# Kernel optimization log

Measured on AMD Instinct MI355X. Metric: run time of the kernel, lower is better.

The kernel has to match this reference:

```python
import jax, jax.numpy as jnp
import numpy as np
import math

# Static config derived from init_kwargs
B, L, D, H, NL = 256, 256, 128, 2, 2
E = D // H                       # 64
F = L // 2 + 1                   # 129 rfft bins
SR = 0.6                         # sample_ratio (> 1/n_layers)
STEP = (F * (1.0 - SR)) // (NL - 1)          # 51.0, python float floor-div as in torch code
LEFTS = [int(F * (1.0 - SR) - k * STEP) for k in range(NL)]   # [51, 0]
RIGHTS = [int(F - k * STEP) for k in range(NL)]               # [129, 78]
TOPK = max(int(1 * math.log(L)), 1)          # factor=1 -> 5
NUM_TOTAL = 100000                           # user_num + item_num
SPATIAL_RATIO = 0.1
INV_SQRT_E = 1.0 / math.sqrt(E)
INV_SQRT_2 = 1.0 / math.sqrt(2.0)


def setup_inputs() -> dict:
    key = jax.random.key(0)
    ks = jax.random.split(key, 12)
    s = 0.05
    return {
        "paths": jax.random.randint(ks[0], (B, L), 0, NUM_TOTAL),
        "lengths": jax.random.randint(ks[1], (B,), 1, L + 1),
        "degrees": jax.random.randint(ks[2], (B,), 0, 64),
        "training": 1,
        "ego_emb": jax.random.normal(ks[3], (NUM_TOTAL + 1, D), jnp.float32) * s,
        "pos_emb": jax.random.normal(ks[4], (L, D), jnp.float32) * s,
        "Wq": jax.random.normal(ks[5], (NL, D, D), jnp.float32) * s,
        "Wk": jax.random.normal(ks[6], (NL, D, D), jnp.float32) * s,
        "Wv": jax.random.normal(ks[7], (NL, D, D), jnp.float32) * s,
        "Wp": jax.random.normal(ks[8], (NL, D, D), jnp.float32) * s,
        "F1": jax.random.normal(ks[9], (NL, D, 2 * D), jnp.float32) * s,
        "F2": jax.random.normal(ks[10], (NL, 2 * D, D), jnp.float32) * s,
    }


def _hybrid_attention(k, x, mask, Wq, Wk, Wv, Wp):
    # project and split heads: [B,H,E,L]
    def proj(W):
        return (x @ W).reshape(B, L, H, E).transpose(0, 2, 3, 1)
    q, kk, v = proj(Wq), proj(Wk), proj(Wv)
    qf = jnp.fft.rfft(q, axis=-1)   # [B,H,E,F] complex
    kf = jnp.fft.rfft(kk, axis=-1)
    vf = jnp.fft.rfft(v, axis=-1)
    l, r = LEFTS[k], RIGHTS[k]
    # frequency-band attention: band-limited cross-correlation (scatter back == zero-pad)
    res = qf[..., l:r] * jnp.conj(kf[..., l:r])
    box = jnp.zeros(qf.shape, dtype=res.dtype).at[..., l:r].set(res)
    corr = jnp.fft.irfft(box, n=L, axis=-1)          # [B,H,E,L]
    mean_value = jnp.mean(corr, axis=(1, 2))         # [B,L]
    # training branch: global topk delays (shared across batch), roll-based aggregation
    _, delays = jax.lax.top_k(jnp.mean(mean_value, axis=0), TOPK)   # [TOPK]
    weights = mean_value[:, delays]                  # [B,TOPK]
    tmp_corr = jax.nn.softmax(weights, axis=-1)      # [B,TOPK]
    # roll(v, -d) along time == gather at (t + d) % L
    idx = (jnp.arange(L)[None, :] + delays[:, None]) % L            # [TOPK,L]
    gathered = v[:, :, :, idx]                       # [B,H,E,TOPK,L]
    freq = jnp.einsum('bhetl,bt->bhel', gathered, tmp_corr)
    freq = freq.transpose(0, 3, 1, 2).reshape(B, L, D)
    # dual-domain: time attention on band-limited signals (std=True -> same band)
    def band_ifft(f):
        padded = jnp.zeros(f.shape, dtype=f.dtype).at[..., l:r].set(f[..., l:r])
        return jnp.fft.irfft(padded, n=L, axis=-1).transpose(0, 1, 3, 2)   # [B,H,L,E]
    qt, kt, vt = band_ifft(qf), band_ifft(kf), band_ifft(vf)
    scores = jnp.einsum('bhqe,bhke->bhqk', qt, kt) * INV_SQRT_E + mask
    att = jax.nn.softmax(scores, axis=-1)
    spatial = jnp.einsum('bhqk,bhke->bhqe', att, vt).transpose(0, 2, 1, 3).reshape(B, L, D)
    out = (1.0 - SPATIAL_RATIO) * freq + SPATIAL_RATIO * spatial
    return out @ Wp + x


def reference(paths, lengths, degrees, training, ego_emb, pos_emb, Wq, Wk, Wv, Wp, F1, F2):
    del degrees, training  # degrees unused; training branch baked in (training=True)
    x = ego_emb[paths] + pos_emb[None, :, :]         # [B,L,D]
    m = (paths < NUM_TOTAL).astype(jnp.float32)
    mask = ((1.0 - m) * -10000.0)[:, None, None, :]  # [B,1,1,L]
    for k in range(NL):
        a = _hybrid_attention(k, x, mask, Wq[k], Wk[k], Wv[k], Wp[k])
        h = a @ F1[k]
        h = h * 0.5 * (1.0 + jax.lax.erf(h * INV_SQRT_2))   # exact GELU
        x = h @ F2[k]
    # gather last valid position per sequence
    return x[jnp.arange(B), lengths - 1]             # [B,D]
```

## Files before the change

kernel.cpp:

```cpp
#include <hip/hip_runtime.h>
#include <math.h>

#define Bn 256
#define Ln 256
#define Dn 128
#define Hn 2
#define En 64
#define NLn 2
#define TOPKn 5
#define NUM_TOTALn 100000
#define BLD (Bn*Ln*Dn)
#define WT_LAYER 147456

using frag_ab = __attribute__((ext_vector_type(8))) short;
using frag_cd = __attribute__((ext_vector_type(4))) float;

__device__ inline short f2bf(float f) {
    union { float f; unsigned u; } c; c.f = f;
    unsigned r = (c.u + 0x7FFFu + ((c.u >> 16) & 1u)) >> 16;
    return (short)r;
}
__device__ inline float bf2f(short s) {
    union { unsigned u; float f; } c; c.u = ((unsigned)(unsigned short)s) << 16;
    return c.f;
}

__global__ void beacon_kernel(float* out, float v) { out[0] = v; }

__global__ __launch_bounds__(256) void build_G_kernel(short* __restrict__ G) {
    int k = blockIdx.x, t = blockIdx.y, s = threadIdx.x;
    int d = (t - s) & 255;
    int f1 = (k == 0) ? 51 : 1;
    int f2 = (k == 0) ? 127 : 77;
    float acc;
    if (d == 0) {
        acc = 2.0f * (float)(f2 - f1 + 1);
    } else {
        const float c = 3.14159265358979323846f / 256.0f;
        int ahi = (d * (2 * f2 + 1)) & 511;
        int alo = (d * (2 * f1 - 1)) & 511;
        acc = (sinf(c * (float)ahi) - sinf(c * (float)alo)) / sinf(c * (float)d);
    }
    acc += (k == 0) ? ((d & 1) ? -1.0f : 1.0f)
                    : 1.0f;
    G[((size_t)k * 256 + t) * 256 + s] = f2bf(acc * (1.0f / 256.0f));
}

__global__ __launch_bounds__(256) void build_x_kernel(const int* __restrict__ paths,
                                                      const float* __restrict__ ego,
                                                      const float* __restrict__ pos,
                                                      short* __restrict__ x) {
    int base = (blockIdx.x * 256 + threadIdx.x) * 4;
    int d = base & 127;
    int bl = base >> 7;
    int t = bl & 255;
    float4 e = *(const float4*)(ego + (size_t)paths[bl] * Dn + d);
    float4 p = *(const float4*)(pos + t * Dn + d);
    short4 s;
    s.x = f2bf(e.x + p.x); s.y = f2bf(e.y + p.y);
    s.z = f2bf(e.z + p.z); s.w = f2bf(e.w + p.w);
    *(short4*)&x[base] = s;
}

__global__ __launch_bounds__(256) void wtrans_all_kernel(
        const float* __restrict__ Wq, const float* __restrict__ Wk,
        const float* __restrict__ Wv, const float* __restrict__ Wp,
        const float* __restrict__ F1, const float* __restrict__ F2,
        short* __restrict__ Wt) {
    int z = blockIdx.y;
    int idx = blockIdx.x * 256 + threadIdx.x;
    short* WtL = Wt + (size_t)z * WT_LAYER;
    if (idx < 65536) {
        int which = idx >> 14, local = idx & 16383;
        const float* src = (which == 0) ? Wq : (which == 1) ? Wk
                         : (which == 2) ? Wv : Wp;
        float scale = (which == 3) ? 0.1f : 1.0f;
        int n = local & 127, k = local >> 7;
        WtL[(which << 14) + n * 128 + k] = f2bf(scale * src[(size_t)z * 16384 + local]);
    } else if (idx < 98304) {
        int local = idx - 65536;
        int n = local & 255, k = local >> 8;
        WtL[65536 + n * 128 + k] = f2bf(F1[(size_t)z * 32768 + local]);
    } else {
        int local = idx - 98304;
        int n = local & 127, k = local >> 7;
        WtL[98304 + n * 256 + k] = f2bf(F2[(size_t)z * 32768 + local]);
    }
}

template<bool BT_FAST, bool GELU_EPI>
__global__ __launch_bounds__(256)
void mfma_gemm_kernel(const short* A, const short* Bp, short* C, const short* R,
                      int K, int lda, int ldb, int ldc, int ldr,
                      long long sA, long long sB, long long sC, long long sR,
                      long long sCsplit, float alpha, float beta) {
    int bz = blockIdx.z;
    A += (size_t)bz * sA; C += (size_t)bz * sC;
    if (R) R += (size_t)bz * sR;
    const short* Bt = Bp + (size_t)bz * sB;
    const int m0 = blockIdx.x * 128, n0 = blockIdx.y * 128;
    int n0c = n0;
    if (sCsplit) { C += (size_t)blockIdx.y * sCsplit; n0c = 0; }
    __shared__ short As[128 * 40];
    __shared__ short Bs[128 * 40];
    int tid = threadIdx.x;
    int lane = tid & 63, wave = tid >> 6;
    int wr = (wave >> 1) * 64, wc = (wave & 1) * 64;
    int l15 = lane & 15, qd = lane >> 4;

    frag_cd zero4 = {0.f, 0.f, 0.f, 0.f};
    frag_cd acc[4][4];
    #pragma unroll
    for (int i = 0; i < 4; i++)
        #pragma unroll
        for (int j = 0; j < 4; j++) acc[i][j] = zero4;

    int arow = tid >> 1, acg = (tid & 1) * 16;
    int bnrow = tid >> 1, bcg = (tid & 1) * 16;
    int bkk = tid & 31, bnb = (tid >> 5) * 16;

    int4 pa0, pa1, pb0, pb1;
    {
        const short* ap = A + (size_t)(m0 + arow) * lda + acg;
        pa0 = *(const int4*)ap; pa1 = *(const int4*)(ap + 8);
        if (BT_FAST) {
            const short* bp = Bt + (size_t)(n0 + bnrow) * ldb + bcg;
            pb0 = *(const int4*)bp; pb1 = *(const int4*)(bp + 8);
        } else {
            const short* bp = Bt + (size_t)bkk * ldb + n0 + bnb;
            pb0 = *(const int4*)bp; pb1 = *(const int4*)(bp + 8);
        }
    }

    for (int k0 = 0; k0 < K; k0 += 32) {
        __syncthreads();
        *(int4*)&As[arow * 40 + acg] = pa0;
        *(int4*)&As[arow * 40 + acg + 8] = pa1;
        if (BT_FAST) {
            *(int4*)&Bs[bnrow * 40 + bcg] = pb0;
            *(int4*)&Bs[bnrow * 40 + bcg + 8] = pb1;
        } else {
            short tmp[16];
            *(int4*)&tmp[0] = pb0; *(int4*)&tmp[8] = pb1;
            #pragma unroll
            for (int i = 0; i < 16; i++) Bs[(bnb + i) * 40 + bkk] = tmp[i];
        }
        __syncthreads();
        if (k0 + 32 < K) {
            const short* ap = A + (size_t)(m0 + arow) * lda + k0 + 32 + acg;
            pa0 = *(const int4*)ap; pa1 = *(const int4*)(ap + 8);
            if (BT_FAST) {
                const short* bp = Bt + (size_t)(n0 + bnrow) * ldb + k0 + 32 + bcg;
                pb0 = *(const int4*)bp; pb1 = *(const int4*)(bp + 8);
            } else {
                const short* bp = Bt + (size_t)(k0 + 32 + bkk) * ldb + n0 + bnb;
                pb0 = *(const int4*)bp; pb1 = *(const int4*)(bp + 8);
            }
        }
        frag_ab af[4], bf[4];
        #pragma unroll
        for (int ms = 0; ms < 4; ms++)
            af[ms] = *(frag_ab*)&As[(wr + ms * 16 + l15) * 40 + qd * 8];
        #pragma unroll
        for (int ns = 0; ns < 4; ns++)
            bf[ns] = *(frag_ab*)&Bs[(wc + ns * 16 + l15) * 40 + qd * 8];
        #pragma unroll
        for (int ms = 0; ms < 4; ms++)
            #pragma unroll
            for (int ns = 0; ns < 4; ns++)
                acc[ms][ns] = __builtin_amdgcn_mfma_f32_16x16x32_bf16(
                    bf[ns], af[ms], acc[ms][ns], 0, 0, 0);
    }
    #pragma unroll
    for (int ms = 0; ms < 4; ms++) {
        int m = m0 + wr + ms * 16 + l15;
        #pragma unroll
        for (int ns = 0; ns < 4; ns++) {
            int nb = wc + ns * 16 + qd * 4;
            float v[4];
            #pragma unroll
            for (int r = 0; r < 4; r++) v[r] = alpha * acc[ms][ns][r];
            if (R) {
                short4 r4 = *(const short4*)&R[(size_t)m * ldr + n0 + nb];
                v[0] += beta * bf2f(r4.x); v[1] += beta * bf2f(r4.y);
                v[2] += beta * bf2f(r4.z); v[3] += beta * bf2f(r4.w);
            }
            if (GELU_EPI) {
                #pragma unroll
                for (int r = 0; r < 4; r++)
                    v[r] = v[r] * 0.5f * (1.0f + erff(v[r] * 0.70710678118654752f));
            }
            short4 o;
            o.x = f2bf(v[0]); o.y = f2bf(v[1]); o.z = f2bf(v[2]); o.w = f2bf(v[3]);
            *(short4*)&C[(size_t)m * ldc + n0c + nb] = o;
        }
    }
}

static inline void mgemm(hipStream_t s, const short* A, const short* B, short* C,
                         const short* R, int M, int N, int K,
                         int lda, int ldb, int ldc, int ldr,
                         long long sA, long long sB, long long sC, long long sR,
                         int batch, float alpha, float beta, bool btFast, bool gelu,
                         long long sCsplit = 0) {
    dim3 grid(M / 128, N / 128, batch), block(256);
    if (btFast) {
        if (gelu) mfma_gemm_kernel<true, true ><<<grid, block, 0, s>>>(A, B, C, R, K, lda, ldb, ldc, ldr, sA, sB, sC, sR, sCsplit, alpha, beta);
        else      mfma_gemm_kernel<true, false><<<grid, block, 0, s>>>(A, B, C, R, K, lda, ldb, ldc, ldr, sA, sB, sC, sR, sCsplit, alpha, beta);
    } else {
        if (gelu) mfma_gemm_kernel<false, true ><<<grid, block, 0, s>>>(A, B, C, R, K, lda, ldb, ldc, ldr, sA, sB, sC, sR, sCsplit, alpha, beta);
        else      mfma_gemm_kernel<false, false><<<grid, block, 0, s>>>(A, B, C, R, K, lda, ldb, ldc, ldr, sA, sB, sC, sR, sCsplit, alpha, beta);
    }
}

__global__ __launch_bounds__(512)
void filtproj_kernel(const short* __restrict__ G, const short* __restrict__ x,
                     const short* __restrict__ W, short* __restrict__ q) {
    int b = blockIdx.x;
    __shared__ short As[256 * 40];
    __shared__ short Bs[128 * 40];
    __shared__ short xf[256 * 136];
    int tid = threadIdx.x;
    int lane = tid & 63, wave = tid >> 6;
    int wr = (wave & 3) * 64, wc = (wave >> 2) * 64;
    int l15 = lane & 15, qd = lane >> 4;
    const short* xb = x + ((size_t)b << 15);

    frag_cd zero4 = {0.f, 0.f, 0.f, 0.f};
    frag_cd acc[4][4];
    #pragma unroll
    for (int i = 0; i < 4; i++)
        #pragma unroll
        for (int j = 0; j < 4; j++) acc[i][j] = zero4;

    int arow = tid >> 1, acg = (tid & 1) * 16;
    int bkk = tid & 31, bnb = (tid >> 5) * 16;

    int4 pa0, pa1, pb0, pb1;
    {
        const short* ap = G + (size_t)arow * 256 + acg;
        pa0 = *(const int4*)ap; pa1 = *(const int4*)(ap + 8);
        if (tid < 256) {
            const short* bp = xb + (size_t)bkk * 128 + bnb;
            pb0 = *(const int4*)bp; pb1 = *(const int4*)(bp + 8);
        }
    }
    for (int k0 = 0; k0 < 256; k0 += 32) {
        __syncthreads();
        *(int4*)&As[arow * 40 + acg] = pa0;
        *(int4*)&As[arow * 40 + acg + 8] = pa1;
        if (tid < 256) {
            short tmp[16];
            *(int4*)&tmp[0] = pb0; *(int4*)&tmp[8] = pb1;
            #pragma unroll
            for (int i = 0; i < 16; i++) Bs[(bnb + i) * 40 + bkk] = tmp[i];
        }
        __syncthreads();
        if (k0 + 32 < 256) {
            const short* ap = G + (size_t)arow * 256 + k0 + 32 + acg;
            pa0 = *(const int4*)ap; pa1 = *(const int4*)(ap + 8);
            if (tid < 256) {
                const short* bp = xb + (size_t)(k0 + 32 + bkk) * 128 + bnb;
                pb0 = *(const int4*)bp; pb1 = *(const int4*)(bp + 8);
            }
        }
        frag_ab af[4], bf[4];
        #pragma unroll
        for (int ms = 0; ms < 4; ms++)
            af[ms] = *(frag_ab*)&As[(wr + ms * 16 + l15) * 40 + qd * 8];
        #pragma unroll
        for (int ns = 0; ns < 4; ns++)
            bf[ns] = *(frag_ab*)&Bs[(wc + ns * 16 + l15) * 40 + qd * 8];
        #pragma unroll
        for (int ms = 0; ms < 4; ms++)
            #pragma unroll
            for (int ns = 0; ns < 4; ns++)
                acc[ms][ns] = __builtin_amdgcn_mfma_f32_16x16x32_bf16(
                    bf[ns], af[ms], acc[ms][ns], 0, 0, 0);
    }
    #pragma unroll
    for (int ms = 0; ms < 4; ms++) {
        int m = wr + ms * 16 + l15;
        #pragma unroll
        for (int ns = 0; ns < 4; ns++) {
            int nb = wc + ns * 16 + qd * 4;
            short4 o;
            o.x = f2bf(acc[ms][ns][0]); o.y = f2bf(acc[ms][ns][1]);
            o.z = f2bf(acc[ms][ns][2]); o.w = f2bf(acc[ms][ns][3]);
            *(short4*)&xf[m * 136 + nb] = o;
        }
    }

    int brow = tid >> 2, bcg = (tid & 3) * 8;
    #pragma unroll 1
    for (int y = 0; y < 3; y++) {
        const short* Bt = W + y * 16384;
        #pragma unroll
        for (int i = 0; i < 4; i++)
            #pragma unroll
            for (int j = 0; j < 4; j++) acc[i][j] = zero4;
        int4 pb = *(const int4*)(Bt + (size_t)brow * 128 + bcg);
        for (int k0 = 0; k0 < 128; k0 += 32) {
            __syncthreads();
            *(int4*)&Bs[brow * 40 + bcg] = pb;
            __syncthreads();
            if (k0 + 32 < 128)
                pb = *(const int4*)(Bt + (size_t)brow * 128 + k0 + 32 + bcg);
            frag_ab af[4], bf[4];
            #pragma unroll
            for (int ms = 0; ms < 4; ms++)
                af[ms] = *(frag_ab*)&xf[(wr + ms * 16 + l15) * 136 + k0 + qd * 8];
            #pragma unroll
            for (int ns = 0; ns < 4; ns++)
                bf[ns] = *(frag_ab*)&Bs[(wc + ns * 16 + l15) * 40 + qd * 8];
            #pragma unroll
            for (int ms = 0; ms < 4; ms++)
                #pragma unroll
                for (int ns = 0; ns < 4; ns++)
                    acc[ms][ns] = __builtin_amdgcn_mfma_f32_16x16x32_bf16(
                        bf[ns], af[ms], acc[ms][ns], 0, 0, 0);
        }
        short* Cy = q + (size_t)y * BLD + ((size_t)b << 15);
        #pragma unroll
        for (int ms = 0; ms < 4; ms++) {
            int m = wr + ms * 16 + l15;
            #pragma unroll
            for (int ns = 0; ns < 4; ns++) {
                int nb = wc + ns * 16 + qd * 4;
                short4 o;
                o.x = f2bf(acc[ms][ns][0]); o.y = f2bf(acc[ms][ns][1]);
                o.z = f2bf(acc[ms][ns][2]); o.w = f2bf(acc[ms][ns][3]);
                *(short4*)&Cy[(size_t)m * 128 + nb] = o;
            }
        }
    }
}

__global__ __launch_bounds__(512)
void amix_ffn_kernel(const short* __restrict__ x, const short* __restrict__ q,
                     const short* __restrict__ W,
                     const float* __restrict__ tc, const int* __restrict__ delays,
                     short* __restrict__ xout) {
    int b = blockIdx.x;
    __shared__ short aL[256 * 132];
    __shared__ short hA[256 * 132];
    __shared__ short Bs[128 * 40];
    short* As = hA;
    int tid = threadIdx.x;
    int lane = tid & 63, wave = tid >> 6;
    int wr = (wave & 3) * 64, wc = (wave >> 2) * 64;
    int l15 = lane & 15, qd = lane >> 4;
    const short* xb = x + ((size_t)b << 15);

    float wj[TOPKn]; int dj[TOPKn];
    #pragma unroll
    for (int j = 0; j < TOPKn; j++) {
        wj[j] = tc[b * TOPKn + j];
        dj[j] = delays[j];
    }

    frag_cd zero4 = {0.f, 0.f, 0.f, 0.f};
    frag_cd acc[4][4];
    #pragma unroll
    for (int i = 0; i < 4; i++)
        #pragma unroll
        for (int j = 0; j < 4; j++) acc[i][j] = zero4;

    int arow = tid >> 1, acg = (tid & 1) * 16;
    int brow = tid >> 2, bcg = (tid & 3) * 8;

    {
        const short* Bt = W + 131072;
        int4 pb0 = *(const int4*)(Bt + (size_t)brow * 128 + bcg);
        for (int k0 = 0; k0 < 128; k0 += 32) {
            __syncthreads();
            #pragma unroll
            for (int c = 0; c < 2; c++) {
                int col = k0 + acg + c * 8;
                float m8[8] = {0.f, 0.f, 0.f, 0.f, 0.f, 0.f, 0.f, 0.f};
                #pragma unroll
                for (int j = 0; j < TOPKn; j++) {
                    frag_ab v = *(const frag_ab*)(xb + (((arow + dj[j]) & 255) << 7) + col);
                    #pragma unroll
                    for (int i = 0; i < 8; i++) m8[i] += wj[j] * bf2f(v[i]);
                }
                frag_ab o;
                #pragma unroll
                for (int i = 0; i < 8; i++) o[i] = f2bf(m8[i]);
                *(frag_ab*)&As[arow * 40 + acg + c * 8] = o;
            }
            *(int4*)&Bs[brow * 40 + bcg] = pb0;
            __syncthreads();
            if (k0 + 32 < 128)
                pb0 = *(const int4*)(Bt + (size_t)brow * 128 + k0 + 32 + bcg);
            frag_ab af[4], bf[4];
            #pragma unroll
            for (int ms = 0; ms < 4; ms++)
                af[ms] = *(frag_ab*)&As[(wr + ms * 16 + l15) * 40 + qd * 8];
            #pragma unroll
            for (int ns = 0; ns < 4; ns++)
                bf[ns] = *(frag_ab*)&Bs[(wc + ns * 16 + l15) * 40 + qd * 8];
            #pragma unroll
            for (int ms = 0; ms < 4; ms++)
                #pragma unroll
                for (int ns = 0; ns < 4; ns++)
                    acc[ms][ns] = __builtin_amdgcn_mfma_f32_16x16x32_bf16(
                        bf[ns], af[ms], acc[ms][ns], 0, 0, 0);
        }
    }
    {
        const short* A2 = q + ((size_t)b << 15);
        const short* Bt = W + 49152;
        int4 pa0, pa1, pb0;
        {
            const short* ap = A2 + (size_t)arow * 128 + acg;
            pa0 = *(const int4*)ap; pa1 = *(const int4*)(ap + 8);
            pb0 = *(const int4*)(Bt + (size_t)brow * 128 + bcg);
        }
        for (int k0 = 0; k0 < 128; k0 += 32) {
            __syncthreads();
            *(int4*)&As[arow * 40 + acg] = pa0;
            *(int4*)&As[arow * 40 + acg + 8] = pa1;
            *(int4*)&Bs[brow * 40 + bcg] = pb0;
            __syncthreads();
            if (k0 + 32 < 128) {
                const short* ap = A2 + (size_t)arow * 128 + k0 + 32 + acg;
                pa0 = *(const int4*)ap; pa1 = *(const int4*)(ap + 8);
                pb0 = *(const int4*)(Bt + (size_t)brow * 128 + k0 + 32 + bcg);
            }
            frag_ab af[4], bf[4];
            #pragma unroll
            for (int ms = 0; ms < 4; ms++)
                af[ms] = *(frag_ab*)&As[(wr + ms * 16 + l15) * 40 + qd * 8];
            #pragma unroll
            for (int ns = 0; ns < 4; ns++)
                bf[ns] = *(frag_ab*)&Bs[(wc + ns * 16 + l15) * 40 + qd * 8];
            #pragma unroll
            for (int ms = 0; ms < 4; ms++)
                #pragma unroll
                for (int ns = 0; ns < 4; ns++)
                    acc[ms][ns] = __builtin_amdgcn_mfma_f32_16x16x32_bf16(
                        bf[ns], af[ms], acc[ms][ns], 0, 0, 0);
        }
    }
    __syncthreads();
    #pragma unroll
    for (int ms = 0; ms < 4; ms++) {
        int m = wr + ms * 16 + l15;
        #pragma unroll
        for (int ns = 0; ns < 4; ns++) {
            int nb = wc + ns * 16 + qd * 4;
            short4 r4 = *(const short4*)&xb[(size_t)m * 128 + nb];
            float v[4];
            v[0] = acc[ms][ns][0] + bf2f(r4.x);
            v[1] = acc[ms][ns][1] + bf2f(r4.y);
            v[2] = acc[ms][ns][2] + bf2f(r4.z);
            v[3] = acc[ms][ns][3] + bf2f(r4.w);
            short4 o;
            o.x = f2bf(v[0]); o.y = f2bf(v[1]); o.z = f2bf(v[2]); o.w = f2bf(v[3]);
            *(short4*)&aL[m * 132 + nb] = o;
        }
    }
    __syncthreads();

    const short* F1T = W + 65536;
    const short* F2T = W + 98304;
    frag_cd xacc[4][4];
    #pragma unroll
    for (int i = 0; i < 4; i++)
        #pragma unroll
        for (int j = 0; j < 4; j++) xacc[i][j] = zero4;

    #pragma unroll 1
    for (int half = 0; half < 2; half++) {
        const short* B1 = F1T + (size_t)(half * 128) * 128;
        frag_cd hacc[4][4];
        #pragma unroll
        for (int i = 0; i < 4; i++)
            #pragma unroll
            for (int j = 0; j < 4; j++) hacc[i][j] = zero4;
        int4 pb = *(const int4*)(B1 + (size_t)brow * 128 + bcg);
        for (int k0 = 0; k0 < 128; k0 += 32) {
            __syncthreads();
            *(int4*)&Bs[brow * 40 + bcg] = pb;
            __syncthreads();
            if (k0 + 32 < 128)
                pb = *(const int4*)(B1 + (size_t)brow * 128 + k0 + 32 + bcg);
            frag_ab af[4], bf[4];
            #pragma unroll
            for (int ms = 0; ms < 4; ms++)
                af[ms] = *(frag_ab*)&aL[(wr + ms * 16 + l15) * 132 + k0 + qd * 8];
            #pragma unroll
            for (int ns = 0; ns < 4; ns++)
                bf[ns] = *(frag_ab*)&Bs[(wc + ns * 16 + l15) * 40 + qd * 8];
            #pragma unroll
            for (int ms = 0; ms < 4; ms++)
                #pragma unroll
                for (int ns = 0; ns < 4; ns++)
                    hacc[ms][ns] = __builtin_amdgcn_mfma_f32_16x16x32_bf16(
                        bf[ns], af[ms], hacc[ms][ns], 0, 0, 0);
        }
        __syncthreads();
        #pragma unroll
        for (int ms = 0; ms < 4; ms++) {
            int m = wr + ms * 16 + l15;
            #pragma unroll
            for (int ns = 0; ns < 4; ns++) {
                int nb = wc + ns * 16 + qd * 4;
                float v[4];
                #pragma unroll
                for (int r = 0; r < 4; r++) {
                    float t = hacc[ms][ns][r];
                    v[r] = t * 0.5f * (1.0f + erff(t * 0.70710678118654752f));
                }
                short4 o;
                o.x = f2bf(v[0]); o.y = f2bf(v[1]);
                o.z = f2bf(v[2]); o.w = f2bf(v[3]);
                *(short4*)&hA[m * 132 + nb] = o;
            }
        }
        __syncthreads();

        int4 pb2 = *(const int4*)(F2T + (size_t)brow * 256 + half * 128 + bcg);
        for (int k0 = 0; k0 < 128; k0 += 32) {
            __syncthreads();
            *(int4*)&Bs[brow * 40 + bcg] = pb2;
            __syncthreads();
            if (k0 + 32 < 128)
                pb2 = *(const int4*)(F2T + (size_t)brow * 256 + half * 128 + k0 + 32 + bcg);
            frag_ab af[4], bf[4];
            #pragma unroll
            for (int ms = 0; ms < 4; ms++)
                af[ms] = *(frag_ab*)&hA[(wr + ms * 16 + l15) * 132 + k0 + qd * 8];
            #pragma unroll
            for (int ns = 0; ns < 4; ns++)
                bf[ns] = *(frag_ab*)&Bs[(wc + ns * 16 + l15) * 40 + qd * 8];
            #pragma unroll
            for (int ms = 0; ms < 4; ms++)
                #pragma unroll
                for (int ns = 0; ns < 4; ns++)
                    xacc[ms][ns] = __builtin_amdgcn_mfma_f32_16x16x32_bf16(
                        bf[ns], af[ms], xacc[ms][ns], 0, 0, 0);
        }
    }
    short* xo = xout + ((size_t)b << 15);
    #pragma unroll
    for (int ms = 0; ms < 4; ms++) {
        int m = wr + ms * 16 + l15;
        #pragma unroll
        for (int ns = 0; ns < 4; ns++) {
            int nb = wc + ns * 16 + qd * 4;
            short4 o;
            o.x = f2bf(xacc[ms][ns][0]); o.y = f2bf(xacc[ms][ns][1]);
            o.z = f2bf(xacc[ms][ns][2]); o.w = f2bf(xacc[ms][ns][3]);
            *(short4*)&xo[(size_t)m * 128 + nb] = o;
        }
    }
}

__global__ __launch_bounds__(512, 4) void attn_kernel(short* q,
        const short* __restrict__ kb, const short* __restrict__ vf,
        const int* __restrict__ paths, float* __restrict__ mv2) {
    int h = blockIdx.x, b = blockIdx.y;
    __shared__ short SB[256 * 72];
    __shared__ short ks[64 * 72];
    __shared__ short vT[80 * 72];
    __shared__ float masks[256];
    __shared__ float mvpart[512];
    int tid = threadIdx.x;
    int lane = tid & 63, wave = tid >> 6;
    int l15 = lane & 15, qd = lane >> 4;
    if (tid < 256) masks[tid] = (paths[b * 256 + tid] < NUM_TOTALn) ? 0.0f : -10000.0f;
    {
        int e0 = tid * 2;
        #pragma unroll
        for (int i = 0; i < 2; i++) {
            int e = e0 + i;
            int row = 64 + (e >> 6), col = e & 63;
            vT[row * 72 + col] = (row == 64) ? (short)0x3F80 : (short)0;
        }
    }
    short* qg = q + ((size_t)b << 15) + (size_t)h * 64;
    const short* kg = kb + ((size_t)b << 15) + (size_t)h * 64;
    const short* vg = vf + ((size_t)b << 15) + (size_t)h * 64;

    #pragma unroll
    for (int p = 0; p < 4; p++) {
        int chunk = p * 512 + tid;
        int r = chunk >> 3, cb = (chunk & 7) * 8;
        *(frag_ab*)&SB[r * 72 + cb] = *(const frag_ab*)(qg + (size_t)r * 128 + cb);
    }
    __syncthreads();
    int myrow = wave * 32;
    frag_ab aq[2][2];
    #pragma unroll
    for (int mt = 0; mt < 2; mt++)
        #pragma unroll
        for (int hf = 0; hf < 2; hf++)
            aq[mt][hf] = *(frag_ab*)&SB[(myrow + mt * 16 + l15) * 72 + hf * 32 + qd * 8];

    frag_cd zero4 = {0.f, 0.f, 0.f, 0.f};
    frag_cd oacc[2][5];
    #pragma unroll
    for (int mt = 0; mt < 2; mt++)
        #pragma unroll
        for (int et = 0; et < 5; et++) oacc[mt][et] = zero4;
    float macc = 0.0f;
    int tau = tid & 255, half = tid >> 8;

    for (int jt = 0; jt < 4; jt++) {
        __syncthreads();
        {
            int r = tid >> 3, cb = (tid & 7) * 8;
            *(frag_ab*)&ks[r * 72 + cb] =
                *(const frag_ab*)(kg + (size_t)(jt * 64 + r) * 128 + cb);
            frag_ab v8 = *(const frag_ab*)(vg + (size_t)(jt * 64 + r) * 128 + cb);
            int swz = (((r >> 3) ^ (cb >> 3)) << 3) + (r & 7);
            #pragma unroll
            for (int i = 0; i < 8; i++) vT[(cb + i) * 72 + swz] = v8[i];
        }
        __syncthreads();
        #pragma unroll
        for (int mt = 0; mt < 2; mt++) {
            #pragma unroll
            for (int nt = 0; nt < 4; nt++) {
                frag_ab b0 = *(frag_ab*)&ks[(nt * 16 + l15) * 72 + qd * 8];
                frag_ab b1 = *(frag_ab*)&ks[(nt * 16 + l15) * 72 + 32 + qd * 8];
                frag_cd c = zero4;
                c = __builtin_amdgcn_mfma_f32_16x16x32_bf16(aq[mt][0], b0, c, 0, 0, 0);
                c = __builtin_amdgcn_mfma_f32_16x16x32_bf16(aq[mt][1], b1, c, 0, 0, 0);
                int keyLocal = nt * 16 + l15;
                #pragma unroll
                for (int r = 0; r < 4; r++) {
                    int row = myrow + mt * 16 + qd * 4 + r;
                    int tt = (row - jt * 64 - keyLocal) & 255;
                    SB[tt * 66 + keyLocal] = f2bf(c[r] * 0.125f);
                }
            }
        }
        __syncthreads();
        {
            const int* SD32 = (const int*)&SB[tau * 66 + half * 32];
            #pragma unroll
            for (int i = 0; i < 16; i++) {
                int pk = SD32[i];
                macc += bf2f((short)(pk & 0xFFFF)) + bf2f((short)(pk >> 16));
            }
        }
        #pragma unroll
        for (int mt = 0; mt < 2; mt++) {
            int row = myrow + mt * 16 + l15;
            #pragma unroll
            for (int hf = 0; hf < 2; hf++) {
                int kl0 = hf * 32 + qd * 8;
                frag_ab pfrag;
                #pragma unroll
                for (int j = 0; j < 8; j++) {
                    int kl = kl0 + j;
                    int tt = (row - jt * 64 - kl) & 255;
                    float s = bf2f(SB[tt * 66 + kl]);
                    pfrag[j] = f2bf(__expf(s + masks[jt * 64 + kl]));
                }
                #pragma unroll
                for (int et = 0; et < 5; et++) {
                    int e = et * 16 + l15;
                    int blk = (hf * 4 + qd) ^ ((e >> 3) & 7);
                    frag_ab bv = *(frag_ab*)&vT[e * 72 + (blk << 3)];
                    oacc[mt][et] = __builtin_amdgcn_mfma_f32_16x16x32_bf16(pfrag, bv, oacc[mt][et], 0, 0, 0);
                }
            }
        }
    }
    __syncthreads();
    mvpart[tid] = macc;
    __syncthreads();
    if (tid < 256)
        mv2[(size_t)h * 65536 + b * 256 + tid] =
            (mvpart[tid] + mvpart[tid + 256]) * 0.0625f;
    #pragma unroll
    for (int mt = 0; mt < 2; mt++) {
        #pragma unroll
        for (int r = 0; r < 4; r++) {
            float l = oacc[mt][4][r];
            l = __shfl(l, (lane & 48));
            float inv = 1.0f / l;
            int row = myrow + mt * 16 + qd * 4 + r;
            #pragma unroll
            for (int et = 0; et < 4; et++)
                qg[(size_t)row * 128 + et * 16 + l15] = f2bf(oacc[mt][et][r] * inv);
        }
    }
}

__global__ __launch_bounds__(256) void gm_reduce_kernel(const float* __restrict__ mv2,
                                                        float* __restrict__ gm) {
    int tau = blockIdx.x;
    int b = threadIdx.x;
    __shared__ float red[256];
    red[b] = mv2[b * 256 + tau] + mv2[65536 + b * 256 + tau];
    __syncthreads();
    for (int s = 128; s > 0; s >>= 1) { if (b < s) red[b] += red[b + s]; __syncthreads(); }
    if (b == 0) gm[tau] = red[0] * (1.0f / 256.0f);
}

__global__ __launch_bounds__(256) void topk_softmax_kernel(const float* __restrict__ gm,
                                                           const float* __restrict__ mv2,
                                                           int* __restrict__ delays,
                                                           float* __restrict__ tc) {
    __shared__ float vsh[4];
    __shared__ int ish[4];
    __shared__ int dsh[TOPKn];
    int tid = threadIdx.x;
    int lane = tid & 63, wave = tid >> 6;
    float v = gm[tid];
    for (int t = 0; t < TOPKn; t++) {
        float mv_ = v; int mi = tid;
        #pragma unroll
        for (int s = 32; s > 0; s >>= 1) {
            float v2 = __shfl_xor(mv_, s); int i2 = __shfl_xor(mi, s);
            if (v2 > mv_ || (v2 == mv_ && i2 < mi)) { mv_ = v2; mi = i2; }
        }
        if (lane == 0) { vsh[wave] = mv_; ish[wave] = mi; }
        __syncthreads();
        if (tid == 0) {
            float bv = vsh[0]; int bi = ish[0];
            #pragma unroll
            for (int w = 1; w < 4; w++)
                if (vsh[w] > bv || (vsh[w] == bv && ish[w] < bi)) { bv = vsh[w]; bi = ish[w]; }
            dsh[t] = bi; delays[t] = bi;
        }
        __syncthreads();
        if (tid == dsh[t]) v = -1e30f;
    }
    __syncthreads();
    int b = tid;
    float w[TOPKn];
    float m = -1e30f;
    #pragma unroll
    for (int j = 0; j < TOPKn; j++) {
        w[j] = mv2[b * 256 + dsh[j]] + mv2[65536 + b * 256 + dsh[j]];
        m = fmaxf(m, w[j]);
    }
    float ssum = 0.0f;
    #pragma unroll
    for (int j = 0; j < TOPKn; j++) { w[j] = expf(w[j] - m); ssum += w[j]; }
    #pragma unroll
    for (int j = 0; j < TOPKn; j++) tc[b * TOPKn + j] = w[j] / ssum;
}

__global__ __launch_bounds__(256) void gather_out_kernel(const short* __restrict__ x,
                                                         const int* __restrict__ lengths,
                                                         float* __restrict__ out) {
    int idx = blockIdx.x * 256 + threadIdx.x;
    int d = idx & 127;
    int b = idx >> 7;
    out[idx] = bf2f(x[((size_t)b << 15) + (size_t)(lengths[b] - 1) * Dn + d]);
}

extern "C" void kernel_launch(void* const* d_in, const int* in_sizes, int n_in,
                              void* d_out, int out_size, void* d_ws, size_t ws_size,
                              hipStream_t stream) {
    const int* paths    = (const int*)d_in[0];
    const int* lengths  = (const int*)d_in[1];
    const float* ego    = (const float*)d_in[4];
    const float* pos    = (const float*)d_in[5];
    const float* Wq     = (const float*)d_in[6];
    const float* Wk     = (const float*)d_in[7];
    const float* Wv     = (const float*)d_in[8];
    const float* Wp     = (const float*)d_in[9];
    const float* F1     = (const float*)d_in[10];
    const float* F2     = (const float*)d_in[11];
    float* out = (float*)d_out;

    const size_t need = (size_t)5 * BLD * 2 + 131072 * 2 + 131072 * 4
                        + 256 * 4 + 1280 * 4 + 16 * 4 + (size_t)NLn * WT_LAYER * 2;
    if (ws_size < need) {
        beacon_kernel<<<dim3(1), dim3(1), 0, stream>>>(out, (float)(ws_size >> 20));
        return;
    }

    short* x    = (short*)d_ws;
    short* q    = x + (size_t)1 * BLD;
    short* kb   = x + (size_t)2 * BLD;
    short* vf   = x + (size_t)3 * BLD;
    short* Gb   = x + (size_t)5 * BLD;
    float* mv   = (float*)(Gb + 131072);
    float* gm   = mv + 131072;
    float* tc   = gm + 256;
    int* delays = (int*)(tc + 1280);
    short* Wt   = (short*)(delays + 16);

    build_G_kernel<<<dim3(2, 256), dim3(256), 0, stream>>>(Gb);
    build_x_kernel<<<dim3(BLD / 1024), dim3(256), 0, stream>>>(paths, ego, pos, x);

    wtrans_all_kernel<<<dim3(512, NLn), dim3(256), 0, stream>>>(Wq, Wk, Wv, Wp, F1, F2, Wt);
    mgemm(stream, Wt + 49152, Wt + 32768, Wt + 131072, nullptr,
          128, 128, 128, 128, 128, 128, 0,
          WT_LAYER, WT_LAYER, WT_LAYER, 0, NLn,
          9.0f, 0.0f, false, false);

    for (int k = 0; k < NLn; k++) {
        const short* WtL = Wt + (size_t)k * WT_LAYER;
        filtproj_kernel<<<dim3(256), dim3(512), 0, stream>>>(
            Gb + (size_t)k * 65536, x, WtL, q);

        attn_kernel<<<dim3(2, 256), dim3(512), 0, stream>>>(q, kb, vf, paths, mv);

        gm_reduce_kernel<<<dim3(256), dim3(256), 0, stream>>>(mv, gm);
        topk_softmax_kernel<<<dim3(1), dim3(256), 0, stream>>>(gm, mv, delays, tc);

        amix_ffn_kernel<<<dim3(256), dim3(512), 0, stream>>>(
            x, q, WtL, tc, delays, x);
    }

    gather_out_kernel<<<dim3((Bn * Dn) / 256), dim3(256), 0, stream>>>(x, lengths, out);
}
```

Baseline: 346.0 us.

## Load GEMM weight fragments directly from global and stage full A tiles once

In the fused attention-mix/FFN kernel, the per-k-step shared-memory staging of weight tiles (Bs) is removed, and MFMA B fragments are read straight from global memory (L2/cache-resident weights). The time-delay-aggregated input and q are computed/copied once into the full-width aL/hA shared buffers before the GEMMs, eliminating the many per-iteration __syncthreads barriers. The trade-off is redundant global weight reads across waves without explicit prefetch, which can expose latency in exchange for less synchronization.

Result: slower. 364.5 us (+5.4%).

```diff
diff --git a/kernel.cpp b/kernel.cpp
--- a/kernel.cpp
+++ b/kernel.cpp
@@ -344,8 +344,6 @@
     int b = blockIdx.x;
     __shared__ short aL[256 * 132];
     __shared__ short hA[256 * 132];
-    __shared__ short Bs[128 * 40];
-    short* As = hA;
     int tid = threadIdx.x;
     int lane = tid & 63, wave = tid >> 6;
     int wr = (wave & 3) * 64, wc = (wave >> 2) * 64;
@@ -360,20 +358,11 @@
     }
 
     frag_cd zero4 = {0.f, 0.f, 0.f, 0.f};
-    frag_cd acc[4][4];
-    #pragma unroll
-    for (int i = 0; i < 4; i++)
-        #pragma unroll
-        for (int j = 0; j < 4; j++) acc[i][j] = zero4;
-
-    int arow = tid >> 1, acg = (tid & 1) * 16;
-    int brow = tid >> 2, bcg = (tid & 3) * 8;
 
     {
-        const short* Bt = W + 131072;
-        int4 pb0 = *(const int4*)(Bt + (size_t)brow * 128 + bcg);
+        int arow = tid >> 1, acg = (tid & 1) * 16;
+        #pragma unroll
         for (int k0 = 0; k0 < 128; k0 += 32) {
-            __syncthreads();
             #pragma unroll
             for (int c = 0; c < 2; c++) {
                 int col = k0 + acg + c * 8;
@@ -387,19 +376,34 @@
                 frag_ab o;
                 #pragma unroll
                 for (int i = 0; i < 8; i++) o[i] = f2bf(m8[i]);
-                *(frag_ab*)&As[arow * 40 + acg + c * 8] = o;
-            }
-            *(int4*)&Bs[brow * 40 + bcg] = pb0;
-            __syncthreads();
-            if (k0 + 32 < 128)
-                pb0 = *(const int4*)(Bt + (size_t)brow * 128 + k0 + 32 + bcg);
+                *(frag_ab*)&hA[arow * 132 + col] = o;
+            }
+        }
+        const short* qb = q + ((size_t)b << 15);
+        #pragma unroll
+        for (int p = 0; p < 8; p++) {
+            int chunk = p * 512 + tid;
+            int r = chunk >> 4, cb = (chunk & 15) * 8;
+            *(frag_ab*)&aL[r * 132 + cb] = *(const frag_ab*)(qb + (size_t)r * 128 + cb);
+        }
+    }
+    __syncthreads();
+
+    frag_cd acc[4][4];
+    #pragma unroll
+    for (int i = 0; i < 4; i++)
+        #pragma unroll
+        for (int j = 0; j < 4; j++) acc[i][j] = zero4;
+    {
+        const short* Bt = W + 131072;
+        for (int k0 = 0; k0 < 128; k0 += 32) {
             frag_ab af[4], bf[4];
             #pragma unroll
             for (int ms = 0; ms < 4; ms++)
-                af[ms] = *(frag_ab*)&As[(wr + ms * 16 + l15) * 40 + qd * 8];
+                af[ms] = *(frag_ab*)&hA[(wr + ms * 16 + l15) * 132 + k0 + qd * 8];
             #pragma unroll
             for (int ns = 0; ns < 4; ns++)
-                bf[ns] = *(frag_ab*)&Bs[(wc + ns * 16 + l15) * 40 + qd * 8];
+                bf[ns] = *(const frag_ab*)(Bt + (size_t)(wc + ns * 16 + l15) * 128 + k0 + qd * 8);
             #pragma unroll
             for (int ms = 0; ms < 4; ms++)
                 #pragma unroll
@@ -409,32 +413,15 @@
         }
     }
     {
-        const short* A2 = q + ((size_t)b << 15);
         const short* Bt = W + 49152;
-        int4 pa0, pa1, pb0;
-        {
-            const short* ap = A2 + (size_t)arow * 128 + acg;
-            pa0 = *(const int4*)ap; pa1 = *(const int4*)(ap + 8);
-            pb0 = *(const int4*)(Bt + (size_t)brow * 128 + bcg);
-        }
         for (int k0 = 0; k0 < 128; k0 += 32) {
-            __syncthreads();
-            *(int4*)&As[arow * 40 + acg] = pa0;
-            *(int4*)&As[arow * 40 + acg + 8] = pa1;
-            *(int4*)&Bs[brow * 40 + bcg] = pb0;
-            __syncthreads();
-            if (k0 + 32 < 128) {
-                const short* ap = A2 + (size_t)arow * 128 + k0 + 32 + acg;
-                pa0 = *(const int4*)ap; pa1 = *(const int4*)(ap + 8);
-                pb0 = *(const int4*)(Bt + (size_t)brow * 128 + k0 + 32 + bcg);
-            }
             frag_ab af[4], bf[4];
             #pragma unroll
             for (int ms = 0; ms < 4; ms++)
-                af[ms] = *(frag_ab*)&As[(wr + ms * 16 + l15) * 40 + qd * 8];
+                af[ms] = *(frag_ab*)&aL[(wr + ms * 16 + l15) * 132 + k0 + qd * 8];
             #pragma unroll
             for (int ns = 0; ns < 4; ns++)
-                bf[ns] = *(frag_ab*)&Bs[(wc + ns * 16 + l15) * 40 + qd * 8];
+                bf[ns] = *(const frag_ab*)(Bt + (size_t)(wc + ns * 16 + l15) * 128 + k0 + qd * 8);
             #pragma unroll
             for (int ms = 0; ms < 4; ms++)
                 #pragma unroll
@@ -479,20 +466,14 @@
         for (int i = 0; i < 4; i++)
             #pragma unroll
             for (int j = 0; j < 4; j++) hacc[i][j] = zero4;
-        int4 pb = *(const int4*)(B1 + (size_t)brow * 128 + bcg);
         for (int k0 = 0; k0 < 128; k0 += 32) {
-            __syncthreads();
-            *(int4*)&Bs[brow * 40 + bcg] = pb;
-            __syncthreads();
-            if (k0 + 32 < 128)
-                pb = *(const int4*)(B1 + (size_t)brow * 128 + k0 + 32 + bcg);
             frag_ab af[4], bf[4];
             #pragma unroll
             for (int ms = 0; ms < 4; ms++)
                 af[ms] = *(frag_ab*)&aL[(wr + ms * 16 + l15) * 132 + k0 + qd * 8];
             #pragma unroll
             for (int ns = 0; ns < 4; ns++)
-                bf[ns] = *(frag_ab*)&Bs[(wc + ns * 16 + l15) * 40 + qd * 8];
+                bf[ns] = *(const frag_ab*)(B1 + (size_t)(wc + ns * 16 + l15) * 128 + k0 + qd * 8);
             #pragma unroll
             for (int ms = 0; ms < 4; ms++)
                 #pragma unroll
@@ -521,20 +502,14 @@
         }
         __syncthreads();
 
-        int4 pb2 = *(const int4*)(F2T + (size_t)brow * 256 + half * 128 + bcg);
         for (int k0 = 0; k0 < 128; k0 += 32) {
-            __syncthreads();
-            *(int4*)&Bs[brow * 40 + bcg] = pb2;
-            __syncthreads();
-            if (k0 + 32 < 128)
-                pb2 = *(const int4*)(F2T + (size_t)brow * 256 + half * 128 + k0 + 32 + bcg);
             frag_ab af[4], bf[4];
             #pragma unroll
             for (int ms = 0; ms < 4; ms++)
                 af[ms] = *(frag_ab*)&hA[(wr + ms * 16 + l15) * 132 + k0 + qd * 8];
             #pragma unroll
             for (int ns = 0; ns < 4; ns++)
-                bf[ns] = *(frag_ab*)&Bs[(wc + ns * 16 + l15) * 40 + qd * 8];
+                bf[ns] = *(const frag_ab*)(F2T + (size_t)(wc + ns * 16 + l15) * 256 + half * 128 + k0 + qd * 8);
             #pragma unroll
             for (int ms = 0; ms < 4; ms++)
                 #pragma unroll
```
